# Optimization experiments

Hardware: AMD Instinct MI355X
Metric: run time of the kernel (lower is better)

The kernel has to match this reference:

```python
import jax, jax.numpy as jnp
import numpy as np

B, D_IN, D_HID, D_OUT, E = 8192, 1024, 4096, 1024, 8


def setup_inputs() -> dict:
    key = jax.random.key(0)
    ks = jax.random.split(key, 6)
    s_in = 1.0 / np.sqrt(D_IN)
    s_gh = 1.0 / np.sqrt(D_HID // 2)
    s_eh = 1.0 / np.sqrt(D_HID)
    return {
        "x": jax.random.normal(ks[0], (B, D_IN), jnp.float32),
        "gW1": jax.random.normal(ks[1], (D_IN, D_HID // 2), jnp.float32) * s_in,
        "gb1": jnp.zeros((D_HID // 2,), jnp.float32),
        "gW2": jax.random.normal(ks[2], (D_HID // 2, E), jnp.float32) * s_gh,
        "gb2": jnp.zeros((E,), jnp.float32),
        "eW1": jax.random.normal(ks[3], (E, D_IN, D_HID), jnp.float32) * s_in,
        "eb1": jnp.zeros((E, D_HID), jnp.float32),
        "eW2": jax.random.normal(ks[4], (E, D_HID, D_OUT), jnp.float32) * s_eh,
        "eb2": jnp.zeros((E, D_OUT), jnp.float32),
    }


def reference(x, gW1, gb1, gW2, gb2, eW1, eb1, eW2, eb2):
    # Gating network: Linear -> ReLU -> (Dropout: eval identity) -> Linear -> Softmax(dim=1)
    gh = jax.nn.relu(x @ gW1 + gb1)                      # [B, H/2]
    gates = jax.nn.softmax(gh @ gW2 + gb2, axis=1)       # [B, E]

    # All experts run on the full batch (dense MoE): batched GEMMs over expert axis.
    h = jax.nn.relu(jnp.einsum('bi,eih->beh', x, eW1) + eb1)   # [B, E, H]
    eo = jnp.einsum('beh,eho->beo', h, eW2) + eb2              # [B, E, O]

    # Gated weighted sum over experts.
    combined = jnp.einsum('beo,be->bo', eo, gates)             # [B, O]
    return (combined, gates, gates)
```

## Files before the change

### kernel.cpp

```cpp
#include <hip/hip_runtime.h>
#include <hip/hip_bf16.h>
#include <stdint.h>

#define BB 8192
#define DIN 1024
#define DHID 4096
#define DOUT 1024
#define NEXP 8
#define GH_N 2048

typedef __attribute__((ext_vector_type(8))) __bf16 bf16x8;
typedef __attribute__((ext_vector_type(4))) float f32x4;

__device__ inline unsigned short f2bf(float f) {
  unsigned u = __builtin_bit_cast(unsigned, f);
  u = (u + 0x7FFFu + ((u >> 16) & 1u)) >> 16;
  return (unsigned short)u;
}
__device__ inline float b2f(unsigned short s) {
  return __builtin_bit_cast(float, (unsigned)s << 16);
}

__global__ void cvt_f32_bf16(const float* __restrict__ in,
                             unsigned short* __restrict__ out, int n4) {
  int i = blockIdx.x * blockDim.x + threadIdx.x;
  if (i >= n4) return;
  float4 v = ((const float4*)in)[i];
  ushort4 o;
  o.x = f2bf(v.x); o.y = f2bf(v.y); o.z = f2bf(v.z); o.w = f2bf(v.w);
  ((ushort4*)out)[i] = o;
}

__global__ void transpose_cvt(const float* __restrict__ in,
                              unsigned short* __restrict__ out, int R, int C) {
  __shared__ float tile[32][33];
  int c0 = blockIdx.x * 32, r0 = blockIdx.y * 32;
  int tx = threadIdx.x & 31, ty = threadIdx.x >> 5;
#pragma unroll
  for (int i = 0; i < 4; ++i)
    tile[ty + i * 8][tx] = in[(size_t)(r0 + ty + i * 8) * C + c0 + tx];
  __syncthreads();
#pragma unroll
  for (int i = 0; i < 4; ++i)
    out[(size_t)(c0 + ty + i * 8) * R + r0 + tx] = f2bf(tile[tx][ty + i * 8]);
}

__device__ inline void gload16(const void* g, void* l) {
  __builtin_amdgcn_global_load_lds(
      (const __attribute__((address_space(1))) void*)g,
      (__attribute__((address_space(3))) void*)l, 16, 0, 0);
}

template <int N>
__device__ inline void waitv() {
  if constexpr (N == 0) asm volatile("s_waitcnt vmcnt(0)" ::: "memory");
  else if constexpr (N == 1) asm volatile("s_waitcnt vmcnt(1)" ::: "memory");
  else if constexpr (N == 2) asm volatile("s_waitcnt vmcnt(2)" ::: "memory");
  else if constexpr (N == 3) asm volatile("s_waitcnt vmcnt(3)" ::: "memory");
  else if constexpr (N == 4) asm volatile("s_waitcnt vmcnt(4)" ::: "memory");
  else asm volatile("s_waitcnt vmcnt(0)" ::: "memory");
}
__device__ inline void waitlgkm0() {
  asm volatile("s_waitcnt lgkmcnt(0)" ::: "memory");
  __builtin_amdgcn_sched_barrier(0);
}
__device__ inline bf16x8 ldr(const char* p) { return *(const bf16x8*)p; }

template <int BM, int EPI>
__global__ __launch_bounds__(512, 2)
void gemmP(const unsigned short* __restrict__ A,
           const unsigned short* __restrict__ Bt,
           int M, int N, int K,
           const float* __restrict__ bias,
           unsigned short* __restrict__ outb,
           float* __restrict__ outf,
           const float* __restrict__ gates,
           int eidx, int accum) {
  constexpr int BN = 256;
  constexpr int WROWS = BM / 2;
  constexpr int RM = WROWS / 16;
  constexpr int HM = RM / 2;
  constexpr int ABYTES = BM * 128;
  constexpr int BBYTES = BN * 128;
  constexpr int AUN = BM / 64;
  constexpr int WS = (BM == 256) ? 4 : 3;
  constexpr int W0L = (BM == 256) ? 2 : 1;

  __shared__ char lds[2 * (ABYTES + BBYTES)];
  char* Als = lds;
  char* Bls = lds + 2 * ABYTES;

  const int t = threadIdx.x;
  const int lane = t & 63;
  const int wid = t >> 6;
  const int wm = wid >> 2;
  const int wn = wid & 3;
  const int l15 = lane & 15, lg = lane >> 4;

  const int nwg = gridDim.x, flat = blockIdx.x;
  const int swz = (flat & 7) * (nwg >> 3) + (flat >> 3);
  const int nbn = N >> 8;
  const int bn = swz % nbn, bm = swz / nbn;
  const int m0 = bm * BM, n0 = bn * BN;

  const int prow = t >> 3;
  const int cOff = ((t & 7) ^ (prow & 7)) * 8;
  const unsigned short* aP[AUN];
  const unsigned short* bP[4];
#pragma unroll
  for (int u = 0; u < AUN; ++u) {
    int p = u * 64 + prow;
    int g;
    if (BM == 256) g = ((p >> 6) & 1) * 128 + ((p >> 7) & 1) * 64 + (p & 63);
    else           g = ((p >> 5) & 1) * 64  + ((p >> 6) & 1) * 32 + (p & 31);
    aP[u] = A + (size_t)(m0 + g) * K + cOff;
  }
#pragma unroll
  for (int u = 0; u < 4; ++u) {
    int p = u * 64 + prow;
    int g = ((p >> 5) & 3) * 64 + ((p >> 7) & 1) * 32 + (p & 31);
    bP[u] = Bt + (size_t)(n0 + g) * K + cOff;
  }
  const int ldst = t * 16;

  const int slot0 = ((lg) ^ (l15 & 7)) * 16;
  const int slot1 = ((4 + lg) ^ (l15 & 7)) * 16;
  const int aRB0 = (0 * (BM / 2) + wm * (WROWS / 2) + l15) * 128;
  const int aRB1 = (1 * (BM / 2) + wm * (WROWS / 2) + l15) * 128;
  const int bCB0 = (0 * (BN / 2) + wn * 32 + l15) * 128;
  const int bCB1 = (1 * (BN / 2) + wn * 32 + l15) * 128;

  f32x4 acc[RM][4];
  const f32x4 zero = {0.f, 0.f, 0.f, 0.f};
#pragma unroll
  for (int i = 0; i < RM; ++i)
#pragma unroll
    for (int j = 0; j < 4; ++j) acc[i][j] = zero;

  bf16x8 ar[HM][2], bc0[2][2], bc1[2][2];

  const int NT = K >> 6;

  {
    gload16(bP[0], Bls + 0 * 8192 + ldst);
    gload16(bP[1], Bls + 1 * 8192 + ldst);
    gload16(aP[0], Als + 0 * 8192 + ldst);
    if (AUN == 4) gload16(aP[1], Als + 1 * 8192 + ldst);
    gload16(bP[2], Bls + 2 * 8192 + ldst);
    gload16(bP[3], Bls + 3 * 8192 + ldst);
    if (AUN == 4) {
      gload16(aP[2], Als + 2 * 8192 + ldst);
      gload16(aP[3], Als + 3 * 8192 + ldst);
    } else {
      gload16(aP[1], Als + 1 * 8192 + ldst);
    }
  }
  waitv<WS>();
  __builtin_amdgcn_s_barrier();

  for (int T = 0; T < NT; ++T) {
    const int buf = T & 1;
    const char* Ab = Als + buf * ABYTES;
    const char* Bb = Bls + buf * BBYTES;
    char* An = Als + (buf ^ 1) * ABYTES;
    char* Bn = Bls + (buf ^ 1) * BBYTES;
    const bool stg = (T + 1 < NT);
    const int kn = (T + 1) << 6;

#pragma unroll
    for (int f = 0; f < HM; ++f) {
      ar[f][0] = ldr(Ab + aRB0 + f * 2048 + slot0);
      ar[f][1] = ldr(Ab + aRB0 + f * 2048 + slot1);
    }
#pragma unroll
    for (int c = 0; c < 2; ++c) {
      bc0[c][0] = ldr(Bb + bCB0 + c * 2048 + slot0);
      bc0[c][1] = ldr(Bb + bCB0 + c * 2048 + slot1);
    }
    if (stg) {
      gload16(bP[0] + kn, Bn + 0 * 8192 + ldst);
      gload16(bP[1] + kn, Bn + 1 * 8192 + ldst);
    }
    __builtin_amdgcn_s_barrier();
    waitlgkm0();
    __builtin_amdgcn_s_setprio(1);
#pragma unroll
    for (int ks = 0; ks < 2; ++ks)
#pragma unroll
      for (int f = 0; f < HM; ++f)
#pragma unroll
        for (int c = 0; c < 2; ++c)
          acc[f][c] = __builtin_amdgcn_mfma_f32_16x16x32_bf16(
              ar[f][ks], bc0[c][ks], acc[f][c], 0, 0, 0);
    __builtin_amdgcn_s_setprio(0);
    if (stg) waitv<WS>(); else waitv<W0L>();
    __builtin_amdgcn_s_barrier();

#pragma unroll
    for (int c = 0; c < 2; ++c) {
      bc1[c][0] = ldr(Bb + bCB1 + c * 2048 + slot0);
      bc1[c][1] = ldr(Bb + bCB1 + c * 2048 + slot1);
    }
    if (stg) {
      gload16(aP[0] + kn, An + 0 * 8192 + ldst);
      if (AUN == 4) gload16(aP[1] + kn, An + 1 * 8192 + ldst);
    }
    __builtin_amdgcn_s_barrier();
    waitlgkm0();
    __builtin_amdgcn_s_setprio(1);
#pragma unroll
    for (int ks = 0; ks < 2; ++ks)
#pragma unroll
      for (int f = 0; f < HM; ++f)
#pragma unroll
        for (int c = 0; c < 2; ++c)
          acc[f][2 + c] = __builtin_amdgcn_mfma_f32_16x16x32_bf16(
              ar[f][ks], bc1[c][ks], acc[f][2 + c], 0, 0, 0);
    __builtin_amdgcn_s_setprio(0);
    if (stg) waitv<WS>(); else waitv<0>();
    __builtin_amdgcn_s_barrier();

#pragma unroll
    for (int f = 0; f < HM; ++f) {
      ar[f][0] = ldr(Ab + aRB1 + f * 2048 + slot0);
      ar[f][1] = ldr(Ab + aRB1 + f * 2048 + slot1);
    }
    if (stg) {
      gload16(bP[2] + kn, Bn + 2 * 8192 + ldst);
      gload16(bP[3] + kn, Bn + 3 * 8192 + ldst);
    }
    __builtin_amdgcn_s_barrier();
    waitlgkm0();
    __builtin_amdgcn_s_setprio(1);
#pragma unroll
    for (int ks = 0; ks < 2; ++ks)
#pragma unroll
      for (int f = 0; f < HM; ++f)
#pragma unroll
        for (int c = 0; c < 2; ++c)
          acc[HM + f][2 + c] = __builtin_amdgcn_mfma_f32_16x16x32_bf16(
              ar[f][ks], bc1[c][ks], acc[HM + f][2 + c], 0, 0, 0);
    __builtin_amdgcn_s_setprio(0);
    __builtin_amdgcn_s_barrier();

    if (stg) {
      if (AUN == 4) {
        gload16(aP[2] + kn, An + 2 * 8192 + ldst);
        gload16(aP[3] + kn, An + 3 * 8192 + ldst);
      } else {
        gload16(aP[1] + kn, An + 1 * 8192 + ldst);
      }
    }
    __builtin_amdgcn_s_barrier();
    __builtin_amdgcn_s_setprio(1);
#pragma unroll
    for (int ks = 0; ks < 2; ++ks)
#pragma unroll
      for (int f = 0; f < HM; ++f)
#pragma unroll
        for (int c = 0; c < 2; ++c)
          acc[HM + f][c] = __builtin_amdgcn_mfma_f32_16x16x32_bf16(
              ar[f][ks], bc0[c][ks], acc[HM + f][c], 0, 0, 0);
    __builtin_amdgcn_s_setprio(0);
    if (stg) waitv<WS>();
    __builtin_amdgcn_s_barrier();
  }

  const int rb = m0 + wm * WROWS + (lg << 2);
  const int cb = n0 + wn * 64 + l15;
  if (EPI == 0) {
#pragma unroll
    for (int fg = 0; fg < RM; ++fg) {
#pragma unroll
      for (int j = 0; j < 4; ++j) {
        int col = cb + j * 16;
        float bv = bias[col];
#pragma unroll
        for (int r = 0; r < 4; ++r) {
          int row = rb + fg * 16 + r;
          float v = acc[fg][j][r] + bv;
          outb[(size_t)row * N + col] = f2bf(fmaxf(v, 0.f));
        }
      }
    }
  } else {
#pragma unroll
    for (int fg = 0; fg < RM; ++fg) {
      float g[4];
#pragma unroll
      for (int r = 0; r < 4; ++r)
        g[r] = gates[(size_t)(rb + fg * 16 + r) * NEXP + eidx];
#pragma unroll
      for (int j = 0; j < 4; ++j) {
        int col = cb + j * 16;
        float bv = bias[col];
#pragma unroll
        for (int r = 0; r < 4; ++r) {
          size_t o = (size_t)(rb + fg * 16 + r) * N + col;
          float v = (acc[fg][j][r] + bv) * g[r];
          outf[o] = accum ? outf[o] + v : v;
        }
      }
    }
  }
}

__global__ __launch_bounds__(512)
void gating_head2(const unsigned short* __restrict__ gh,
                  const float* __restrict__ gW2,
                  const float* __restrict__ gb2,
                  float* __restrict__ gws,
                  float* __restrict__ g1,
                  float* __restrict__ g2) {
  __shared__ float wT[8][2048];
  const int t = threadIdx.x;
  for (int idx = t; idx < 16384; idx += 512) {
    wT[idx & 7][idx >> 3] = gW2[idx];
  }
  __syncthreads();
  const int wid = t >> 6, lane = t & 63;
  const int row = blockIdx.x * 8 + wid;
  const unsigned short* ghr = gh + (size_t)row * 2048;
  float s[8] = {0.f, 0.f, 0.f, 0.f, 0.f, 0.f, 0.f, 0.f};
#pragma unroll
  for (int j = 0; j < 8; ++j) {
    int k4 = lane + 64 * j;
    ushort4 hv = ((const ushort4*)ghr)[k4];
    float h0 = b2f(hv.x), h1 = b2f(hv.y), h2 = b2f(hv.z), h3 = b2f(hv.w);
#pragma unroll
    for (int e = 0; e < 8; ++e) {
      float4 w = ((const float4*)&wT[e][0])[k4];
      s[e] += h0 * w.x + h1 * w.y + h2 * w.z + h3 * w.w;
    }
  }
#pragma unroll
  for (int e = 0; e < 8; ++e)
#pragma unroll
    for (int off = 1; off < 64; off <<= 1) s[e] += __shfl_xor(s[e], off, 64);
  if (lane == 0) {
    float l[8], m = -1e30f;
#pragma unroll
    for (int e = 0; e < 8; ++e) {
      l[e] = s[e] + gb2[e];
      m = fmaxf(m, l[e]);
    }
    float sum = 0.f;
#pragma unroll
    for (int e = 0; e < 8; ++e) {
      l[e] = expf(l[e] - m);
      sum += l[e];
    }
    float inv = 1.f / sum;
#pragma unroll
    for (int e = 0; e < 8; ++e) {
      float gv = l[e] * inv;
      gws[(size_t)row * 8 + e] = gv;
      g1[(size_t)row * 8 + e] = gv;
      g2[(size_t)row * 8 + e] = gv;
    }
  }
}

extern "C" void kernel_launch(void* const* d_in, const int* in_sizes, int n_in,
                              void* d_out, int out_size, void* d_ws,
                              size_t ws_size, hipStream_t stream) {
  (void)in_sizes; (void)n_in; (void)out_size; (void)ws_size;
  const float* x   = (const float*)d_in[0];
  const float* gW1 = (const float*)d_in[1];
  const float* gb1 = (const float*)d_in[2];
  const float* gW2 = (const float*)d_in[3];
  const float* gb2 = (const float*)d_in[4];
  const float* eW1 = (const float*)d_in[5];
  const float* eb1 = (const float*)d_in[6];
  const float* eW2 = (const float*)d_in[7];
  const float* eb2 = (const float*)d_in[8];

  float* outC  = (float*)d_out;
  float* outG1 = outC + (size_t)BB * DOUT;
  float* outG2 = outG1 + (size_t)BB * NEXP;

  char* ws = (char*)d_ws;
  unsigned short* xb   = (unsigned short*)(ws);
  unsigned short* gW1T = (unsigned short*)(ws + 16777216);
  unsigned short* gh   = (unsigned short*)(ws + 20971520);
  float*          gat  = (float*)(ws + 54525952);
  unsigned short* w1T  = (unsigned short*)(ws + 54788096);
  unsigned short* w2T  = (unsigned short*)(ws + 63176704);
  unsigned short* hbuf = (unsigned short*)(ws + 71565312);

  cvt_f32_bf16<<<(BB * DIN / 4) / 256, 256, 0, stream>>>(x, xb, BB * DIN / 4);
  transpose_cvt<<<dim3(GH_N / 32, DIN / 32), 256, 0, stream>>>(gW1, gW1T, DIN, GH_N);
  gemmP<256, 0><<<dim3((BB / 256) * (GH_N / 256)), 512, 0, stream>>>(
      xb, gW1T, BB, GH_N, DIN, gb1, gh, nullptr, nullptr, 0, 0);
  gating_head2<<<BB / 8, 512, 0, stream>>>(gh, gW2, gb2, gat, outG1, outG2);

  for (int e = 0; e < NEXP; ++e) {
    transpose_cvt<<<dim3(DHID / 32, DIN / 32), 256, 0, stream>>>(
        eW1 + (size_t)e * DIN * DHID, w1T, DIN, DHID);
    transpose_cvt<<<dim3(DOUT / 32, DHID / 32), 256, 0, stream>>>(
        eW2 + (size_t)e * DHID * DOUT, w2T, DHID, DOUT);
    gemmP<256, 0><<<dim3((BB / 256) * (DHID / 256)), 512, 0, stream>>>(
        xb, w1T, BB, DHID, DIN, eb1 + (size_t)e * DHID, hbuf, nullptr, nullptr, 0, 0);
    gemmP<128, 1><<<dim3((BB / 128) * (DOUT / 256)), 512, 0, stream>>>(
        hbuf, w2T, BB, DOUT, DHID, eb2 + (size_t)e * DOUT, nullptr, outC, gat, e, e > 0);
  }
}
```

Measured before the change: 1.416 ms.

## Split-K second expert GEMM with BM=256 tiles and deferred gated combine

The second expert GEMM now uses 256-row tiles split into two K halves. The halves write fp32 partials to workspace, and the next expert's first GEMM folds them into the output (bias, gate and accumulate) in its epilogue, with a final combine kernel for the last expert. The two per-expert weight transposes are merged into one launch. The aim is to raise occupancy and tile efficiency of the small-N second GEMM and cut launches. The cost is extra fp32 partial traffic, a serial combine loop done by only the bn==0 blocks, and a dependence on a larger workspace, with the old path kept as a fallback.

```diff
diff --git a/kernel.cpp b/kernel.cpp
--- a/kernel.cpp
+++ b/kernel.cpp
@@ -31,10 +31,11 @@
   ((ushort4*)out)[i] = o;
 }
 
-__global__ void transpose_cvt(const float* __restrict__ in,
-                              unsigned short* __restrict__ out, int R, int C) {
+__device__ inline void tr_tile(const float* __restrict__ in,
+                               unsigned short* __restrict__ out, int R, int C,
+                               int bx, int by) {
   __shared__ float tile[32][33];
-  int c0 = blockIdx.x * 32, r0 = blockIdx.y * 32;
+  int c0 = bx * 32, r0 = by * 32;
   int tx = threadIdx.x & 31, ty = threadIdx.x >> 5;
 #pragma unroll
   for (int i = 0; i < 4; ++i)
@@ -43,6 +44,24 @@
 #pragma unroll
   for (int i = 0; i < 4; ++i)
     out[(size_t)(c0 + ty + i * 8) * R + r0 + tx] = f2bf(tile[tx][ty + i * 8]);
+}
+
+__global__ void transpose_cvt(const float* __restrict__ in,
+                              unsigned short* __restrict__ out, int R, int C) {
+  tr_tile(in, out, R, C, blockIdx.x, blockIdx.y);
+}
+
+__global__ void transpose_cvt2(const float* __restrict__ w1,
+                               unsigned short* __restrict__ w1T,
+                               const float* __restrict__ w2,
+                               unsigned short* __restrict__ w2T) {
+  int b = blockIdx.x;
+  if (b < 4096) {
+    tr_tile(w1, w1T, DIN, DHID, b & 127, b >> 7);
+  } else {
+    b -= 4096;
+    tr_tile(w2, w2T, DHID, DOUT, b & 31, b >> 5);
+  }
 }
 
 __device__ inline void gload16(const void* g, void* l) {
@@ -68,14 +87,15 @@
 
 template <int BM, int EPI>
 __global__ __launch_bounds__(512, 2)
-void gemmP(const unsigned short* __restrict__ A,
-           const unsigned short* __restrict__ Bt,
+void gemmP(const unsigned short* __restrict__ A, int lda,
+           const unsigned short* __restrict__ Bt, int ldb,
            int M, int N, int K,
            const float* __restrict__ bias,
            unsigned short* __restrict__ outb,
            float* __restrict__ outf,
-           const float* __restrict__ gates,
-           int eidx, int accum) {
+           const float* __restrict__ gates, int eidx, int accum,
+           const float* __restrict__ comb0, const float* __restrict__ comb1,
+           const float* __restrict__ combBias) {
   constexpr int BN = 256;
   constexpr int WROWS = BM / 2;
   constexpr int RM = WROWS / 16;
@@ -99,9 +119,13 @@
 
   const int nwg = gridDim.x, flat = blockIdx.x;
   const int swz = (flat & 7) * (nwg >> 3) + (flat >> 3);
+  int ks = 0, tid = swz;
+  if (EPI == 2) { ks = swz & 1; tid = swz >> 1; }
   const int nbn = N >> 8;
-  const int bn = swz % nbn, bm = swz / nbn;
+  const int bn = tid % nbn, bm = tid / nbn;
   const int m0 = bm * BM, n0 = bn * BN;
+  const int kbase = ks * K;
+  if (EPI == 2) outf += (size_t)ks * ((size_t)M * N);
 
   const int prow = t >> 3;
   const int cOff = ((t & 7) ^ (prow & 7)) * 8;
@@ -113,13 +137,13 @@
     int g;
     if (BM == 256) g = ((p >> 6) & 1) * 128 + ((p >> 7) & 1) * 64 + (p & 63);
     else           g = ((p >> 5) & 1) * 64  + ((p >> 6) & 1) * 32 + (p & 31);
-    aP[u] = A + (size_t)(m0 + g) * K + cOff;
+    aP[u] = A + (size_t)(m0 + g) * lda + kbase + cOff;
   }
 #pragma unroll
   for (int u = 0; u < 4; ++u) {
     int p = u * 64 + prow;
     int g = ((p >> 5) & 3) * 64 + ((p >> 7) & 1) * 32 + (p & 31);
-    bP[u] = Bt + (size_t)(n0 + g) * K + cOff;
+    bP[u] = Bt + (size_t)(n0 + g) * ldb + kbase + cOff;
   }
   const int ldst = t * 16;
 
@@ -185,13 +209,13 @@
     waitlgkm0();
     __builtin_amdgcn_s_setprio(1);
 #pragma unroll
-    for (int ks = 0; ks < 2; ++ks)
+    for (int ksl = 0; ksl < 2; ++ksl)
 #pragma unroll
       for (int f = 0; f < HM; ++f)
 #pragma unroll
         for (int c = 0; c < 2; ++c)
           acc[f][c] = __builtin_amdgcn_mfma_f32_16x16x32_bf16(
-              ar[f][ks], bc0[c][ks], acc[f][c], 0, 0, 0);
+              ar[f][ksl], bc0[c][ksl], acc[f][c], 0, 0, 0);
     __builtin_amdgcn_s_setprio(0);
     if (stg) waitv<WS>(); else waitv<W0L>();
     __builtin_amdgcn_s_barrier();
@@ -209,13 +233,13 @@
     waitlgkm0();
     __builtin_amdgcn_s_setprio(1);
 #pragma unroll
-    for (int ks = 0; ks < 2; ++ks)
+    for (int ksl = 0; ksl < 2; ++ksl)
 #pragma unroll
       for (int f = 0; f < HM; ++f)
 #pragma unroll
         for (int c = 0; c < 2; ++c)
           acc[f][2 + c] = __builtin_amdgcn_mfma_f32_16x16x32_bf16(
-              ar[f][ks], bc1[c][ks], acc[f][2 + c], 0, 0, 0);
+              ar[f][ksl], bc1[c][ksl], acc[f][2 + c], 0, 0, 0);
     __builtin_amdgcn_s_setprio(0);
     if (stg) waitv<WS>(); else waitv<0>();
     __builtin_amdgcn_s_barrier();
@@ -233,13 +257,13 @@
     waitlgkm0();
     __builtin_amdgcn_s_setprio(1);
 #pragma unroll
-    for (int ks = 0; ks < 2; ++ks)
+    for (int ksl = 0; ksl < 2; ++ksl)
 #pragma unroll
       for (int f = 0; f < HM; ++f)
 #pragma unroll
         for (int c = 0; c < 2; ++c)
           acc[HM + f][2 + c] = __builtin_amdgcn_mfma_f32_16x16x32_bf16(
-              ar[f][ks], bc1[c][ks], acc[HM + f][2 + c], 0, 0, 0);
+              ar[f][ksl], bc1[c][ksl], acc[HM + f][2 + c], 0, 0, 0);
     __builtin_amdgcn_s_setprio(0);
     __builtin_amdgcn_s_barrier();
 
@@ -254,13 +278,13 @@
     __builtin_amdgcn_s_barrier();
     __builtin_amdgcn_s_setprio(1);
 #pragma unroll
-    for (int ks = 0; ks < 2; ++ks)
+    for (int ksl = 0; ksl < 2; ++ksl)
 #pragma unroll
       for (int f = 0; f < HM; ++f)
 #pragma unroll
         for (int c = 0; c < 2; ++c)
           acc[HM + f][c] = __builtin_amdgcn_mfma_f32_16x16x32_bf16(
-              ar[f][ks], bc0[c][ks], acc[HM + f][c], 0, 0, 0);
+              ar[f][ksl], bc0[c][ksl], acc[HM + f][c], 0, 0, 0);
     __builtin_amdgcn_s_setprio(0);
     if (stg) waitv<WS>();
     __builtin_amdgcn_s_barrier();
@@ -283,7 +307,28 @@
         }
       }
     }
-  } else {
+    if (comb0 != nullptr && bn == 0) {
+      for (int i = 0; i < 128; ++i) {
+        int f = t + i * 512;
+        int r = f >> 8, c4 = f & 255;
+        size_t ro = (size_t)(m0 + r);
+        float g = gates[ro * NEXP + eidx];
+        float4 a = ((const float4*)(comb0 + ro * DOUT))[c4];
+        float4 b = ((const float4*)(comb1 + ro * DOUT))[c4];
+        float4 bb = ((const float4*)combBias)[c4];
+        float4 o;
+        o.x = g * (a.x + b.x + bb.x);
+        o.y = g * (a.y + b.y + bb.y);
+        o.z = g * (a.z + b.z + bb.z);
+        o.w = g * (a.w + b.w + bb.w);
+        if (accum) {
+          float4 p = ((const float4*)(outf + ro * DOUT))[c4];
+          o.x += p.x; o.y += p.y; o.z += p.z; o.w += p.w;
+        }
+        ((float4*)(outf + ro * DOUT))[c4] = o;
+      }
+    }
+  } else if (EPI == 1) {
 #pragma unroll
     for (int fg = 0; fg < RM; ++fg) {
       float g[4];
@@ -302,7 +347,40 @@
         }
       }
     }
-  }
+  } else {
+#pragma unroll
+    for (int fg = 0; fg < RM; ++fg) {
+#pragma unroll
+      for (int j = 0; j < 4; ++j) {
+        int col = cb + j * 16;
+#pragma unroll
+        for (int r = 0; r < 4; ++r) {
+          size_t o = (size_t)(rb + fg * 16 + r) * N + col;
+          outf[o] = acc[fg][j][r];
+        }
+      }
+    }
+  }
+}
+
+__global__ void combine_k(const float* __restrict__ p0,
+                          const float* __restrict__ p1,
+                          const float* __restrict__ bias,
+                          const float* __restrict__ gates, int eidx,
+                          float* __restrict__ outC) {
+  int i = blockIdx.x * blockDim.x + threadIdx.x;
+  int r = i >> 8, c4 = i & 255;
+  float g = gates[(size_t)r * NEXP + eidx];
+  float4 a = ((const float4*)(p0 + (size_t)r * DOUT))[c4];
+  float4 b = ((const float4*)(p1 + (size_t)r * DOUT))[c4];
+  float4 bb = ((const float4*)bias)[c4];
+  float4 p = ((const float4*)(outC + (size_t)r * DOUT))[c4];
+  float4 o;
+  o.x = p.x + g * (a.x + b.x + bb.x);
+  o.y = p.y + g * (a.y + b.y + bb.y);
+  o.z = p.z + g * (a.z + b.z + bb.z);
+  o.w = p.w + g * (a.w + b.w + bb.w);
+  ((float4*)(outC + (size_t)r * DOUT))[c4] = o;
 }
 
 __global__ __launch_bounds__(512)
@@ -364,7 +442,7 @@
 extern "C" void kernel_launch(void* const* d_in, const int* in_sizes, int n_in,
                               void* d_out, int out_size, void* d_ws,
                               size_t ws_size, hipStream_t stream) {
-  (void)in_sizes; (void)n_in; (void)out_size; (void)ws_size;
+  (void)in_sizes; (void)n_in; (void)out_size;
   const float* x   = (const float*)d_in[0];
   const float* gW1 = (const float*)d_in[1];
   const float* gb1 = (const float*)d_in[2];
@@ -381,27 +459,43 @@
 
   char* ws = (char*)d_ws;
   unsigned short* xb   = (unsigned short*)(ws);
-  unsigned short* gW1T = (unsigned short*)(ws + 16777216);
-  unsigned short* gh   = (unsigned short*)(ws + 20971520);
-  float*          gat  = (float*)(ws + 54525952);
-  unsigned short* w1T  = (unsigned short*)(ws + 54788096);
-  unsigned short* w2T  = (unsigned short*)(ws + 63176704);
-  unsigned short* hbuf = (unsigned short*)(ws + 71565312);
+  float*          gat  = (float*)(ws + 16777216);
+  unsigned short* w1T  = (unsigned short*)(ws + 17039360);
+  unsigned short* w2T  = (unsigned short*)(ws + 25427968);
+  unsigned short* hbuf = (unsigned short*)(ws + 33816576);
+  unsigned short* gh   = (unsigned short*)(ws + 100925440);
+  unsigned short* gW1T = (unsigned short*)(ws + 134479872);
+  float*          p0   = (float*)(ws + 100925440);
+  float*          p1   = (float*)(ws + 134479872);
+  const bool splitk = ws_size >= (size_t)168034304;
 
   cvt_f32_bf16<<<(BB * DIN / 4) / 256, 256, 0, stream>>>(x, xb, BB * DIN / 4);
   transpose_cvt<<<dim3(GH_N / 32, DIN / 32), 256, 0, stream>>>(gW1, gW1T, DIN, GH_N);
   gemmP<256, 0><<<dim3((BB / 256) * (GH_N / 256)), 512, 0, stream>>>(
-      xb, gW1T, BB, GH_N, DIN, gb1, gh, nullptr, nullptr, 0, 0);
+      xb, DIN, gW1T, DIN, BB, GH_N, DIN, gb1, gh, nullptr, nullptr, 0, 0,
+      nullptr, nullptr, nullptr);
   gating_head2<<<BB / 8, 512, 0, stream>>>(gh, gW2, gb2, gat, outG1, outG2);
 
   for (int e = 0; e < NEXP; ++e) {
-    transpose_cvt<<<dim3(DHID / 32, DIN / 32), 256, 0, stream>>>(
-        eW1 + (size_t)e * DIN * DHID, w1T, DIN, DHID);
-    transpose_cvt<<<dim3(DOUT / 32, DHID / 32), 256, 0, stream>>>(
-        eW2 + (size_t)e * DHID * DOUT, w2T, DHID, DOUT);
+    transpose_cvt2<<<8192, 256, 0, stream>>>(
+        eW1 + (size_t)e * DIN * DHID, w1T, eW2 + (size_t)e * DHID * DOUT, w2T);
+    const bool comb = splitk && (e > 0);
     gemmP<256, 0><<<dim3((BB / 256) * (DHID / 256)), 512, 0, stream>>>(
-        xb, w1T, BB, DHID, DIN, eb1 + (size_t)e * DHID, hbuf, nullptr, nullptr, 0, 0);
-    gemmP<128, 1><<<dim3((BB / 128) * (DOUT / 256)), 512, 0, stream>>>(
-        hbuf, w2T, BB, DOUT, DHID, eb2 + (size_t)e * DOUT, nullptr, outC, gat, e, e > 0);
-  }
-}
+        xb, DIN, w1T, DIN, BB, DHID, DIN, eb1 + (size_t)e * DHID, hbuf, outC,
+        gat, e - 1, (e - 1) > 0 ? 1 : 0,
+        comb ? p0 : nullptr, p1, eb2 + (size_t)(e > 0 ? e - 1 : 0) * DOUT);
+    if (splitk) {
+      gemmP<256, 2><<<dim3((BB / 256) * (DOUT / 256) * 2), 512, 0, stream>>>(
+          hbuf, DHID, w2T, DHID, BB, DOUT, DHID / 2, nullptr, nullptr, p0,
+          nullptr, 0, 0, nullptr, nullptr, nullptr);
+    } else {
+      gemmP<128, 1><<<dim3((BB / 128) * (DOUT / 256)), 512, 0, stream>>>(
+          hbuf, DHID, w2T, DHID, BB, DOUT, DHID, eb2 + (size_t)e * DOUT,
+          nullptr, outC, gat, e, e > 0 ? 1 : 0, nullptr, nullptr, nullptr);
+    }
+  }
+  if (splitk) {
+    combine_k<<<(BB * DOUT / 4) / 256, 256, 0, stream>>>(
+        p0, p1, eb2 + (size_t)7 * DOUT, gat, 7, outC);
+  }
+}
```

After: 1.723 ms. 1.22x slower.
